# Performance work log

Hardware: AMD Instinct MI355X
Metric: run time of the kernel (lower is better)

## Reference

```python
import jax, jax.numpy as jnp
import numpy as np

B, H, W, C = 8, 96, 96, 512
M, D, K = 128, 256, 300


def _make_norm_adj(rng):
    A = (rng.random((M, M)) < 0.1).astype(np.float32)
    A = np.maximum(A, A.T)
    A = A + np.eye(M, dtype=np.float32)
    d = A.sum(axis=1)
    d_inv_sqrt = np.power(d, -0.5)
    d_inv_sqrt[np.isinf(d_inv_sqrt)] = 0.0
    Dm = np.diag(d_inv_sqrt)
    return (Dm @ A @ Dm).astype(np.float32)


def setup_inputs() -> dict:
    key = jax.random.key(0)
    ks = jax.random.split(key, 12)
    rng = np.random.default_rng(0)
    norm_adj = jnp.asarray(_make_norm_adj(rng))
    word_emb = jnp.asarray(rng.standard_normal((M, K)).astype(np.float32))
    s = lambda fan_in: 1.0 / np.sqrt(fan_in)
    return {
        "x": jax.random.normal(ks[0], (B, H, W, C), jnp.float32),
        "norm_adj": norm_adj,
        "word_emb": word_emb,
        "Wv": jax.random.normal(ks[1], (C, M), jnp.float32) * s(C),   # voting 1x1 conv
        "bv": jnp.zeros((M,), jnp.float32),
        "Wt": jax.random.normal(ks[2], (C, D), jnp.float32) * s(C),   # feat 1x1 conv
        "bt": jnp.zeros((D,), jnp.float32),
        "Wg": jax.random.normal(ks[3], (D + K, D), jnp.float32) * s(D + K),  # gcn dense
        "bg": jnp.zeros((D,), jnp.float32),
        "Wql": jax.random.normal(ks[4], (C, D), jnp.float32) * s(C),  # compat_local (no bias)
        "Wkn": jax.random.normal(ks[5], (D, D), jnp.float32) * s(D),  # compat_node (no bias)
        "Wm": jax.random.normal(ks[6], (D, C), jnp.float32) * s(D),   # map_back
        "bm": jnp.zeros((C,), jnp.float32),
    }


def reference(x, norm_adj, word_emb, Wv, bv, Wt, bt, Wg, bg, Wql, Wkn, Wm, bm):
    b, h, w, c = x.shape
    xf = x.reshape(b, h * w, c)                      # [B, N, C], N = H*W
    # 1) Voting: local features -> semantic nodes
    vote = jax.nn.softmax(xf @ Wv + bv, axis=2)      # [B, N, M]
    local = xf @ Wt + bt                             # [B, N, D]
    node = jnp.einsum('bnm,bnd->bmd', vote, local)   # [B, M, D]
    # 2) Reason: GCN over semantic graph
    emb = jnp.broadcast_to(word_emb[None], (b, M, K))
    gcn_in = jnp.concatenate([node, emb], axis=-1)   # [B, M, D+K]
    gcn = gcn_in @ Wg + bg                           # [B, M, D]
    evolved = jax.nn.relu(jnp.einsum('mk,bkd->bmd', norm_adj, gcn))
    # 3) Project back via cross-attention
    query = xf @ Wql                                 # [B, N, D]
    keyv = evolved @ Wkn                             # [B, M, D]
    attn = jax.nn.softmax(jnp.einsum('bnd,bmd->bnm', query, keyv), axis=-1)
    values = evolved @ Wm + bm                       # [B, M, C]
    out_global = jnp.einsum('bnm,bmc->bnc', attn, values).reshape(b, h, w, c)
    return jax.nn.relu(x + out_global)
```

## Files before the change

### kernel.cpp

```cpp
#include <hip/hip_runtime.h>
#include <hip/hip_bf16.h>

#define BB 8
#define NN 9216
#define BN 73728
#define CC 512
#define MM 128
#define DD 256
#define KK 300
#define DK 556
#define PS 384

typedef __attribute__((ext_vector_type(8))) __bf16 bf16x8;
typedef __attribute__((ext_vector_type(4))) __bf16 bf16x4;
typedef __attribute__((ext_vector_type(4))) float f32x4;

__device__ __forceinline__ void lds_load16(const void* g, void* l) {
    __builtin_amdgcn_global_load_lds(
        (const __attribute__((address_space(1))) unsigned int*)g,
        (__attribute__((address_space(3))) unsigned int*)l, 16, 0, 0);
}

__device__ __forceinline__ bf16x8 combine8(bf16x4 a, bf16x4 b) {
    bf16x8 r;
    r[0] = a[0]; r[1] = a[1]; r[2] = a[2]; r[3] = a[3];
    r[4] = b[0]; r[5] = b[1]; r[6] = b[2]; r[7] = b[3];
    return r;
}

__global__ __launch_bounds__(256) void pack_wt(const float* __restrict__ Wv, const float* __restrict__ bv,
                                               const float* __restrict__ Wt, const float* __restrict__ bt,
                                               const float* __restrict__ Wql,
                                               __bf16* __restrict__ WcatT, float* __restrict__ bias) {
    int gid = blockIdx.x * 256 + threadIdx.x;
    if (gid < 640 * 512) {
        int n = gid >> 9, k = gid & 511;
        float v;
        if (n < 128)       v = Wv[k * 128 + n];
        else if (n < 384)  v = Wt[k * 256 + (n - 128)];
        else               v = Wql[k * 256 + (n - 384)];
        WcatT[gid] = (__bf16)v;
    }
    if (gid < 640) {
        bias[gid] = (gid < 128) ? bv[gid] : ((gid < 384) ? bt[gid - 128] : 0.0f);
    }
}

__global__ __launch_bounds__(256) void cast_x(const float* __restrict__ x, __bf16* __restrict__ xb) {
    long total = (long)BN * CC;
    for (long i = ((long)blockIdx.x * 256 + threadIdx.x) * 8; i < total; i += (long)gridDim.x * 256 * 8) {
        float4 a = *(const float4*)&x[i];
        float4 b = *(const float4*)&x[i + 4];
        bf16x8 o;
        o[0] = (__bf16)a.x; o[1] = (__bf16)a.y; o[2] = (__bf16)a.z; o[3] = (__bf16)a.w;
        o[4] = (__bf16)b.x; o[5] = (__bf16)b.y; o[6] = (__bf16)b.z; o[7] = (__bf16)b.w;
        *(bf16x8*)&xb[i] = o;
    }
}

__global__ __launch_bounds__(256, 2) void proj_mfma(const __bf16* __restrict__ xb,
                                                    const __bf16* __restrict__ WcatT,
                                                    const float* __restrict__ bias,
                                                    float* __restrict__ P,
                                                    __bf16* __restrict__ localbf) {
    __shared__ __align__(16) __bf16 Al[128 * 64];
    __shared__ __align__(16) __bf16 Bl[128 * 64];
    int t = threadIdx.x, w = t >> 6, l = t & 63;
    int lo = l & 15, hi = l >> 4;
    int wr = w >> 1, wc = w & 1;
    int n0 = blockIdx.x * 128;
    long row0 = (long)blockIdx.y * 128;

    f32x4 acc[4][4];
    #pragma unroll
    for (int m = 0; m < 4; m++)
        #pragma unroll
        for (int n = 0; n < 4; n++) acc[m][n] = (f32x4){0.f, 0.f, 0.f, 0.f};

    int lrow = l >> 3, lcol = (l & 7) * 8;
    for (int k0 = 0; k0 < 512; k0 += 64) {
        __syncthreads();
        #pragma unroll
        for (int i = 0; i < 4; i++) {
            int c = w * 4 + i;
            lds_load16(xb + (row0 + c * 8 + lrow) * (long)CC + k0 + lcol,
                       (char*)Al + c * 1024);
            lds_load16(WcatT + (long)(n0 + c * 8 + lrow) * CC + k0 + lcol,
                       (char*)Bl + c * 1024);
        }
        __syncthreads();
        #pragma unroll
        for (int ks = 0; ks < 2; ks++) {
            bf16x8 af[4], bfr[4];
            #pragma unroll
            for (int m = 0; m < 4; m++)
                af[m] = *(const bf16x8*)&Al[(wr * 64 + m * 16 + lo) * 64 + ks * 32 + hi * 8];
            #pragma unroll
            for (int n = 0; n < 4; n++)
                bfr[n] = *(const bf16x8*)&Bl[(wc * 64 + n * 16 + lo) * 64 + ks * 32 + hi * 8];
            #pragma unroll
            for (int m = 0; m < 4; m++)
                #pragma unroll
                for (int n = 0; n < 4; n++)
                    acc[m][n] = __builtin_amdgcn_mfma_f32_16x16x32_bf16(af[m], bfr[n], acc[m][n], 0, 0, 0);
        }
    }

    float bv[4];
    #pragma unroll
    for (int n = 0; n < 4; n++) bv[n] = bias[n0 + wc * 64 + n * 16 + lo];
    #pragma unroll
    for (int m = 0; m < 4; m++)
        #pragma unroll
        for (int n = 0; n < 4; n++)
            #pragma unroll
            for (int r = 0; r < 4; r++) {
                long row = row0 + wr * 64 + m * 16 + hi * 4 + r;
                int col = n0 + wc * 64 + n * 16 + lo;
                float v = acc[m][n][r] + bv[n];
                if (n0 == 0)           P[row * PS + col] = v;
                else if (n0 < 384)     localbf[row * 256 + (col - 128)] = (__bf16)v;
                else                   P[row * PS + (col - 256)] = v;
            }
}

__global__ __launch_bounds__(256) void softmax_vote(const float* __restrict__ P, __bf16* __restrict__ votebf) {
    int wid = threadIdx.x >> 6, lane = threadIdx.x & 63;
    long row = (long)blockIdx.x * 4 + wid;
    const float* p = &P[row * PS];
    float v0 = p[lane], v1 = p[lane + 64];
    float mx = fmaxf(v0, v1);
    #pragma unroll
    for (int off = 32; off; off >>= 1) mx = fmaxf(mx, __shfl_xor(mx, off));
    float e0 = __expf(v0 - mx), e1 = __expf(v1 - mx);
    float s = e0 + e1;
    #pragma unroll
    for (int off = 32; off; off >>= 1) s += __shfl_xor(s, off);
    float r = 1.0f / s;
    votebf[row * 128 + lane] = (__bf16)(e0 * r);
    votebf[row * 128 + lane + 64] = (__bf16)(e1 * r);
}

__global__ __launch_bounds__(256) void node_mfma(const __bf16* __restrict__ votebf,
                                                 const __bf16* __restrict__ localbf,
                                                 float* __restrict__ node) {
    __shared__ __align__(16) __bf16 Vl[128][68];
    __shared__ __align__(16) __bf16 Ll[256][68];
    int t = threadIdx.x, w = t >> 6, l = t & 63;
    int lo = l & 15, hi = l >> 4;
    int b = blockIdx.x / 36, slice = blockIdx.x % 36;
    long base = (long)b * NN + slice * 256;

    f32x4 acc[8][4];
    #pragma unroll
    for (int mt = 0; mt < 8; mt++)
        #pragma unroll
        for (int dt = 0; dt < 4; dt++) acc[mt][dt] = (f32x4){0.f, 0.f, 0.f, 0.f};

    int mcol = t & 127, qh = t >> 7;
    for (int c0 = 0; c0 < 256; c0 += 64) {
        __syncthreads();
        #pragma unroll
        for (int j = 0; j < 8; j++) {
            int q = j * 2 + qh;
            long n = base + c0 + q * 4;
            bf16x4 pk;
            pk[0] = votebf[n * 128 + mcol];
            pk[1] = votebf[(n + 1) * 128 + mcol];
            pk[2] = votebf[(n + 2) * 128 + mcol];
            pk[3] = votebf[(n + 3) * 128 + mcol];
            *(bf16x4*)&Vl[mcol][q * 4] = pk;
        }
        #pragma unroll
        for (int q = 0; q < 16; q++) {
            long n = base + c0 + q * 4;
            bf16x4 pk;
            pk[0] = localbf[n * 256 + t];
            pk[1] = localbf[(n + 1) * 256 + t];
            pk[2] = localbf[(n + 2) * 256 + t];
            pk[3] = localbf[(n + 3) * 256 + t];
            *(bf16x4*)&Ll[t][q * 4] = pk;
        }
        __syncthreads();
        #pragma unroll
        for (int ks = 0; ks < 2; ks++) {
            bf16x8 bfr[4];
            #pragma unroll
            for (int dt = 0; dt < 4; dt++)
                bfr[dt] = combine8(*(const bf16x4*)&Ll[w * 64 + dt * 16 + lo][ks * 32 + hi * 8],
                                   *(const bf16x4*)&Ll[w * 64 + dt * 16 + lo][ks * 32 + hi * 8 + 4]);
            #pragma unroll
            for (int mt = 0; mt < 8; mt++) {
                bf16x8 A = combine8(*(const bf16x4*)&Vl[mt * 16 + lo][ks * 32 + hi * 8],
                                    *(const bf16x4*)&Vl[mt * 16 + lo][ks * 32 + hi * 8 + 4]);
                #pragma unroll
                for (int dt = 0; dt < 4; dt++)
                    acc[mt][dt] = __builtin_amdgcn_mfma_f32_16x16x32_bf16(A, bfr[dt], acc[mt][dt], 0, 0, 0);
            }
        }
    }
    #pragma unroll
    for (int mt = 0; mt < 8; mt++)
        #pragma unroll
        for (int dt = 0; dt < 4; dt++)
            #pragma unroll
            for (int r = 0; r < 4; r++)
                unsafeAtomicAdd(&node[((long)b * MM + mt * 16 + hi * 4 + r) * DD + w * 64 + dt * 16 + lo],
                                acc[mt][dt][r]);
}

__global__ __launch_bounds__(256) void gcn_dense(const float* __restrict__ node, const float* __restrict__ emb,
                                                 const float* __restrict__ Wg, const float* __restrict__ bg,
                                                 float* __restrict__ gcn) {
    __shared__ float a[DK];
    int b = blockIdx.x >> 7, m = blockIdx.x & 127, t = threadIdx.x;
    for (int i = t; i < DK; i += 256)
        a[i] = (i < DD) ? node[(b * MM + m) * DD + i] : emb[m * KK + (i - DD)];
    __syncthreads();
    float acc = bg[t];
    for (int k = 0; k < DK; k++) acc += a[k] * Wg[k * DD + t];
    gcn[(b * MM + m) * DD + t] = acc;
}

__global__ __launch_bounds__(256) void gcn_adj_relu(const float* __restrict__ adj, const float* __restrict__ gcn,
                                                    float* __restrict__ evo) {
    __shared__ float ar[128];
    int b = blockIdx.x >> 7, m = blockIdx.x & 127, t = threadIdx.x;
    if (t < 128) ar[t] = adj[m * MM + t];
    __syncthreads();
    float acc = 0.0f;
    for (int k = 0; k < MM; k++) acc += ar[k] * gcn[(b * MM + k) * DD + t];
    evo[(b * MM + m) * DD + t] = fmaxf(acc, 0.0f);
}

__global__ __launch_bounds__(256) void keyv_k(const float* __restrict__ evo, const float* __restrict__ Wkn,
                                              __bf16* __restrict__ Kbf) {
    __shared__ float e[DD];
    int b = blockIdx.x >> 7, m = blockIdx.x & 127, t = threadIdx.x;
    e[t] = evo[(b * MM + m) * DD + t];
    __syncthreads();
    float acc = 0.0f;
    for (int k = 0; k < DD; k++) acc += e[k] * Wkn[k * DD + t];
    Kbf[(b * MM + m) * DD + t] = (__bf16)acc;
}

__global__ __launch_bounds__(512) void values_k(const float* __restrict__ evo, const float* __restrict__ Wm,
                                                const float* __restrict__ bm, __bf16* __restrict__ Vt) {
    __shared__ float e[DD];
    int b = blockIdx.x >> 7, m = blockIdx.x & 127, t = threadIdx.x;
    if (t < DD) e[t] = evo[(b * MM + m) * DD + t];
    __syncthreads();
    float acc = bm[t];
    for (int k = 0; k < DD; k++) acc += e[k] * Wm[k * CC + t];
    Vt[((long)b * CC + t) * MM + m] = (__bf16)acc;
}

__global__ __launch_bounds__(256, 2) void attn_mfma(const float* __restrict__ P,
                                                    const __bf16* __restrict__ Kbf,
                                                    const __bf16* __restrict__ Vt,
                                                    const float* __restrict__ x,
                                                    float* __restrict__ out) {
    __shared__ __align__(16) __bf16 Pl[4][16][136];
    int t = threadIdx.x;
    int w = t >> 6, l = t & 63;
    int lo = l & 15, hi = l >> 4;
    int b = blockIdx.x / 144, tile = blockIdx.x % 144;
    int n0 = tile * 64;
    long brow = (long)b * NN;
    long qrow = brow + n0 + w * 16 + lo;
    const float* Pq = P + qrow * PS + 128;
    const __bf16* Kb = Kbf + (long)b * MM * DD;
    const __bf16* Vb = Vt + (long)b * CC * MM;

    f32x4 S[8];
    #pragma unroll
    for (int i = 0; i < 8; i++) S[i] = (f32x4){0.f, 0.f, 0.f, 0.f};

    #pragma unroll
    for (int k0 = 0; k0 < 8; k0++) {
        float4 qa = *(const float4*)(Pq + k0 * 32 + hi * 8);
        float4 qb = *(const float4*)(Pq + k0 * 32 + hi * 8 + 4);
        bf16x8 A;
        A[0] = (__bf16)qa.x; A[1] = (__bf16)qa.y; A[2] = (__bf16)qa.z; A[3] = (__bf16)qa.w;
        A[4] = (__bf16)qb.x; A[5] = (__bf16)qb.y; A[6] = (__bf16)qb.z; A[7] = (__bf16)qb.w;
        #pragma unroll
        for (int mt = 0; mt < 8; mt++) {
            bf16x8 Bf = *(const bf16x8*)(Kb + (mt * 16 + lo) * DD + k0 * 32 + hi * 8);
            S[mt] = __builtin_amdgcn_mfma_f32_16x16x32_bf16(A, Bf, S[mt], 0, 0, 0);
        }
    }

    float mx[4], sm[4], rs[4];
    #pragma unroll
    for (int r = 0; r < 4; r++) {
        float m0 = S[0][r];
        #pragma unroll
        for (int mt = 1; mt < 8; mt++) m0 = fmaxf(m0, S[mt][r]);
        #pragma unroll
        for (int off = 1; off < 16; off <<= 1) m0 = fmaxf(m0, __shfl_xor(m0, off));
        mx[r] = m0;
    }
    #pragma unroll
    for (int r = 0; r < 4; r++) sm[r] = 0.f;
    #pragma unroll
    for (int mt = 0; mt < 8; mt++)
        #pragma unroll
        for (int r = 0; r < 4; r++) {
            float e = __expf(S[mt][r] - mx[r]);
            S[mt][r] = e;
            sm[r] += e;
        }
    #pragma unroll
    for (int r = 0; r < 4; r++) {
        float s0 = sm[r];
        #pragma unroll
        for (int off = 1; off < 16; off <<= 1) s0 += __shfl_xor(s0, off);
        rs[r] = 1.0f / s0;
    }
    #pragma unroll
    for (int mt = 0; mt < 8; mt++)
        #pragma unroll
        for (int r = 0; r < 4; r++)
            Pl[w][hi * 4 + r][mt * 16 + lo] = (__bf16)(S[mt][r] * rs[r]);

    f32x4 O[32];
    #pragma unroll
    for (int i = 0; i < 32; i++) O[i] = (f32x4){0.f, 0.f, 0.f, 0.f};

    #pragma unroll
    for (int mc = 0; mc < 4; mc++) {
        bf16x8 A2 = *(const bf16x8*)&Pl[w][lo][mc * 32 + hi * 8];
        #pragma unroll
        for (int ct = 0; ct < 32; ct++) {
            bf16x8 Bv = *(const bf16x8*)(Vb + (long)(ct * 16 + lo) * MM + mc * 32 + hi * 8);
            O[ct] = __builtin_amdgcn_mfma_f32_16x16x32_bf16(A2, Bv, O[ct], 0, 0, 0);
        }
    }

    #pragma unroll
    for (int ct = 0; ct < 32; ct++) {
        #pragma unroll
        for (int r = 0; r < 4; r++) {
            long gi = (brow + n0 + w * 16 + hi * 4 + r) * (long)CC + ct * 16 + lo;
            out[gi] = fmaxf(x[gi] + O[ct][r], 0.f);
        }
    }
}

extern "C" void kernel_launch(void* const* d_in, const int* in_sizes, int n_in,
                              void* d_out, int out_size, void* d_ws, size_t ws_size,
                              hipStream_t stream) {
    const float* x    = (const float*)d_in[0];
    const float* adj  = (const float*)d_in[1];
    const float* emb  = (const float*)d_in[2];
    const float* Wv   = (const float*)d_in[3];
    const float* bv   = (const float*)d_in[4];
    const float* Wt   = (const float*)d_in[5];
    const float* bt   = (const float*)d_in[6];
    const float* Wg   = (const float*)d_in[7];
    const float* bg   = (const float*)d_in[8];
    const float* Wql  = (const float*)d_in[9];
    const float* Wkn  = (const float*)d_in[10];
    const float* Wm   = (const float*)d_in[11];
    const float* bm   = (const float*)d_in[12];
    float* out = (float*)d_out;

    float* ws      = (float*)d_ws;
    __bf16* WcatT  = (__bf16*)ws;
    float* bias    = (float*)(WcatT + 640 * 512);
    float* P       = bias + 640;
    __bf16* localbf = (__bf16*)(P + (long)BN * PS);
    __bf16* votebf  = localbf + (long)BN * 256;
    float* node    = (float*)(votebf + (long)BN * 128);
    float* gcn     = node + BB * MM * DD;
    float* evo     = gcn + BB * MM * DD;
    __bf16* Kbf    = (__bf16*)(evo + BB * MM * DD);
    __bf16* Vt     = Kbf + (long)BB * MM * DD;
    __bf16* xb     = (__bf16*)d_out;

    pack_wt<<<1280, 256, 0, stream>>>(Wv, bv, Wt, bt, Wql, WcatT, bias);
    cast_x<<<2048, 256, 0, stream>>>(x, xb);
    proj_mfma<<<dim3(5, 576), 256, 0, stream>>>(xb, WcatT, bias, P, localbf);
    softmax_vote<<<BN / 4, 256, 0, stream>>>(P, votebf);
    hipMemsetAsync(node, 0, (size_t)BB * MM * DD * sizeof(float), stream);
    node_mfma<<<BB * 36, 256, 0, stream>>>(votebf, localbf, node);
    gcn_dense<<<BB * MM, 256, 0, stream>>>(node, emb, Wg, bg, gcn);
    gcn_adj_relu<<<BB * MM, 256, 0, stream>>>(adj, gcn, evo);
    keyv_k<<<BB * MM, 256, 0, stream>>>(evo, Wkn, Kbf);
    values_k<<<BB * MM, 512, 0, stream>>>(evo, Wm, bm, Vt);
    attn_mfma<<<BB * 144, 256, 0, stream>>>(P, Kbf, Vt, x, out);
}
```

Before: 694.9 us.

## Fuse vote softmax into projection epilogue and split attention output loop

The voting softmax now runs in the projection GEMM epilogue for the first column block, using cross-lane shuffles and shared-memory reductions across the two column warps, and writes bf16 votes directly. This removes the softmax_vote kernel and the fp32 round trip of 128 vote logits per row, so P shrinks to hold only the query columns. The attention kernel splits its 512-channel output accumulation into two halves to cut register pressure and raises launch bounds to 4 blocks per SM for higher occupancy. The trade-off is extra synchronisation and exp work in one projection block column, and the attention loop becomes serial over the two halves.

```diff
diff --git a/kernel.cpp b/kernel.cpp
--- a/kernel.cpp
+++ b/kernel.cpp
@@ -9,7 +9,7 @@
 #define DD 256
 #define KK 300
 #define DK 556
-#define PS 384
+#define PS 256
 
 typedef __attribute__((ext_vector_type(8))) __bf16 bf16x8;
 typedef __attribute__((ext_vector_type(4))) __bf16 bf16x4;
@@ -62,7 +62,8 @@
                                                     const __bf16* __restrict__ WcatT,
                                                     const float* __restrict__ bias,
                                                     float* __restrict__ P,
-                                                    __bf16* __restrict__ localbf) {
+                                                    __bf16* __restrict__ localbf,
+                                                    __bf16* __restrict__ votebf) {
     __shared__ __align__(16) __bf16 Al[128 * 64];
     __shared__ __align__(16) __bf16 Bl[128 * 64];
     int t = threadIdx.x, w = t >> 6, l = t & 63;
@@ -106,39 +107,68 @@
         }
     }
 
-    float bv[4];
-    #pragma unroll
-    for (int n = 0; n < 4; n++) bv[n] = bias[n0 + wc * 64 + n * 16 + lo];
-    #pragma unroll
-    for (int m = 0; m < 4; m++)
-        #pragma unroll
-        for (int n = 0; n < 4; n++)
+    float bv4[4];
+    #pragma unroll
+    for (int n = 0; n < 4; n++) bv4[n] = bias[n0 + wc * 64 + n * 16 + lo];
+
+    if (n0 == 0) {
+        __shared__ float RedM[128][2];
+        __shared__ float RedS[128][2];
+        float gmax[4][4], gsum[4][4];
+        #pragma unroll
+        for (int m = 0; m < 4; m++)
             #pragma unroll
             for (int r = 0; r < 4; r++) {
-                long row = row0 + wr * 64 + m * 16 + hi * 4 + r;
-                int col = n0 + wc * 64 + n * 16 + lo;
-                float v = acc[m][n][r] + bv[n];
-                if (n0 == 0)           P[row * PS + col] = v;
-                else if (n0 < 384)     localbf[row * 256 + (col - 128)] = (__bf16)v;
-                else                   P[row * PS + (col - 256)] = v;
-            }
-}
-
-__global__ __launch_bounds__(256) void softmax_vote(const float* __restrict__ P, __bf16* __restrict__ votebf) {
-    int wid = threadIdx.x >> 6, lane = threadIdx.x & 63;
-    long row = (long)blockIdx.x * 4 + wid;
-    const float* p = &P[row * PS];
-    float v0 = p[lane], v1 = p[lane + 64];
-    float mx = fmaxf(v0, v1);
-    #pragma unroll
-    for (int off = 32; off; off >>= 1) mx = fmaxf(mx, __shfl_xor(mx, off));
-    float e0 = __expf(v0 - mx), e1 = __expf(v1 - mx);
-    float s = e0 + e1;
-    #pragma unroll
-    for (int off = 32; off; off >>= 1) s += __shfl_xor(s, off);
-    float r = 1.0f / s;
-    votebf[row * 128 + lane] = (__bf16)(e0 * r);
-    votebf[row * 128 + lane + 64] = (__bf16)(e1 * r);
+                float pm = acc[m][0][r] + bv4[0];
+                #pragma unroll
+                for (int n = 1; n < 4; n++) pm = fmaxf(pm, acc[m][n][r] + bv4[n]);
+                #pragma unroll
+                for (int off = 1; off < 16; off <<= 1) pm = fmaxf(pm, __shfl_xor(pm, off));
+                gmax[m][r] = pm;
+                RedM[wr * 64 + m * 16 + hi * 4 + r][wc] = pm;
+            }
+        __syncthreads();
+        #pragma unroll
+        for (int m = 0; m < 4; m++)
+            #pragma unroll
+            for (int r = 0; r < 4; r++) {
+                int rl = wr * 64 + m * 16 + hi * 4 + r;
+                gmax[m][r] = fmaxf(RedM[rl][0], RedM[rl][1]);
+                float ps = 0.f;
+                #pragma unroll
+                for (int n = 0; n < 4; n++) ps += __expf(acc[m][n][r] + bv4[n] - gmax[m][r]);
+                #pragma unroll
+                for (int off = 1; off < 16; off <<= 1) ps += __shfl_xor(ps, off);
+                gsum[m][r] = ps;
+                RedS[rl][wc] = ps;
+            }
+        __syncthreads();
+        #pragma unroll
+        for (int m = 0; m < 4; m++)
+            #pragma unroll
+            for (int r = 0; r < 4; r++) {
+                int rl = wr * 64 + m * 16 + hi * 4 + r;
+                float rinv = 1.0f / (RedS[rl][0] + RedS[rl][1]);
+                long grow = row0 + rl;
+                #pragma unroll
+                for (int n = 0; n < 4; n++)
+                    votebf[grow * 128 + wc * 64 + n * 16 + lo] =
+                        (__bf16)(__expf(acc[m][n][r] + bv4[n] - gmax[m][r]) * rinv);
+            }
+    } else {
+        #pragma unroll
+        for (int m = 0; m < 4; m++)
+            #pragma unroll
+            for (int n = 0; n < 4; n++)
+                #pragma unroll
+                for (int r = 0; r < 4; r++) {
+                    long row = row0 + wr * 64 + m * 16 + hi * 4 + r;
+                    int col = n0 + wc * 64 + n * 16 + lo;
+                    float v = acc[m][n][r] + bv4[n];
+                    if (n0 < 384) localbf[row * 256 + (col - 128)] = (__bf16)v;
+                    else          P[row * PS + (col - 384)] = v;
+                }
+    }
 }
 
 __global__ __launch_bounds__(256) void node_mfma(const __bf16* __restrict__ votebf,
@@ -255,7 +285,7 @@
     Vt[((long)b * CC + t) * MM + m] = (__bf16)acc;
 }
 
-__global__ __launch_bounds__(256, 2) void attn_mfma(const float* __restrict__ P,
+__global__ __launch_bounds__(256, 4) void attn_mfma(const float* __restrict__ P,
                                                     const __bf16* __restrict__ Kbf,
                                                     const __bf16* __restrict__ Vt,
                                                     const float* __restrict__ x,
@@ -268,7 +298,7 @@
     int n0 = tile * 64;
     long brow = (long)b * NN;
     long qrow = brow + n0 + w * 16 + lo;
-    const float* Pq = P + qrow * PS + 128;
+    const float* Pq = P + qrow * PS;
     const __bf16* Kb = Kbf + (long)b * MM * DD;
     const __bf16* Vb = Vt + (long)b * CC * MM;
 
@@ -323,26 +353,27 @@
         for (int r = 0; r < 4; r++)
             Pl[w][hi * 4 + r][mt * 16 + lo] = (__bf16)(S[mt][r] * rs[r]);
 
-    f32x4 O[32];
-    #pragma unroll
-    for (int i = 0; i < 32; i++) O[i] = (f32x4){0.f, 0.f, 0.f, 0.f};
-
-    #pragma unroll
-    for (int mc = 0; mc < 4; mc++) {
-        bf16x8 A2 = *(const bf16x8*)&Pl[w][lo][mc * 32 + hi * 8];
-        #pragma unroll
-        for (int ct = 0; ct < 32; ct++) {
-            bf16x8 Bv = *(const bf16x8*)(Vb + (long)(ct * 16 + lo) * MM + mc * 32 + hi * 8);
-            O[ct] = __builtin_amdgcn_mfma_f32_16x16x32_bf16(A2, Bv, O[ct], 0, 0, 0);
-        }
-    }
-
-    #pragma unroll
-    for (int ct = 0; ct < 32; ct++) {
-        #pragma unroll
-        for (int r = 0; r < 4; r++) {
-            long gi = (brow + n0 + w * 16 + hi * 4 + r) * (long)CC + ct * 16 + lo;
-            out[gi] = fmaxf(x[gi] + O[ct][r], 0.f);
+    #pragma unroll 1
+    for (int c2 = 0; c2 < 2; c2++) {
+        f32x4 O[16];
+        #pragma unroll
+        for (int i = 0; i < 16; i++) O[i] = (f32x4){0.f, 0.f, 0.f, 0.f};
+        #pragma unroll
+        for (int mc = 0; mc < 4; mc++) {
+            bf16x8 A2 = *(const bf16x8*)&Pl[w][lo][mc * 32 + hi * 8];
+            #pragma unroll
+            for (int ct = 0; ct < 16; ct++) {
+                bf16x8 Bv = *(const bf16x8*)(Vb + (long)(c2 * 256 + ct * 16 + lo) * MM + mc * 32 + hi * 8);
+                O[ct] = __builtin_amdgcn_mfma_f32_16x16x32_bf16(A2, Bv, O[ct], 0, 0, 0);
+            }
+        }
+        #pragma unroll
+        for (int ct = 0; ct < 16; ct++) {
+            #pragma unroll
+            for (int r = 0; r < 4; r++) {
+                long gi = (brow + n0 + w * 16 + hi * 4 + r) * (long)CC + c2 * 256 + ct * 16 + lo;
+                out[gi] = fmaxf(x[gi] + O[ct][r], 0.f);
+            }
         }
     }
 }
@@ -380,8 +411,7 @@
 
     pack_wt<<<1280, 256, 0, stream>>>(Wv, bv, Wt, bt, Wql, WcatT, bias);
     cast_x<<<2048, 256, 0, stream>>>(x, xb);
-    proj_mfma<<<dim3(5, 576), 256, 0, stream>>>(xb, WcatT, bias, P, localbf);
-    softmax_vote<<<BN / 4, 256, 0, stream>>>(P, votebf);
+    proj_mfma<<<dim3(5, 576), 256, 0, stream>>>(xb, WcatT, bias, P, localbf, votebf);
     hipMemsetAsync(node, 0, (size_t)BB * MM * DD * sizeof(float), stream);
     node_mfma<<<BB * 36, 256, 0, stream>>>(votebf, localbf, node);
     gcn_dense<<<BB * MM, 256, 0, stream>>>(node, emb, Wg, bg, gcn);
```

Measured after the change: 810.3 us. 16.6% more time.
